# Kernel tuning notes

Hardware: AMD Instinct MI355X
Metric: run time of the kernel (lower is better)

## Reference

```python
import jax, jax.numpy as jnp
import numpy as np

D_MODEL = 1024
NUM_HEADS = 16
D_K = D_MODEL // NUM_HEADS
B, S = 2, 2048
NEG = -1e9


def setup_inputs() -> dict:
    key = jax.random.key(0)
    ks = jax.random.split(key, 12)
    scale = 1.0 / np.sqrt(D_MODEL)
    inp = {
        'q': jax.random.normal(ks[0], (B, S, D_MODEL), jnp.float32),
        'k': jax.random.normal(ks[1], (B, S, D_MODEL), jnp.float32),
        'v': jax.random.normal(ks[2], (B, S, D_MODEL), jnp.float32),
        'mask': jax.random.randint(ks[3], (1, 1, S, S), 0, 2, jnp.int32),
        'wq_w': jax.random.normal(ks[4], (D_MODEL, D_MODEL), jnp.float32) * scale,
        'wq_b': jnp.zeros((D_MODEL,), jnp.float32),
        'wk_w': jax.random.normal(ks[5], (D_MODEL, D_MODEL), jnp.float32) * scale,
        'wk_b': jnp.zeros((D_MODEL,), jnp.float32),
        'wv_w': jax.random.normal(ks[6], (D_MODEL, D_MODEL), jnp.float32) * scale,
        'wv_b': jnp.zeros((D_MODEL,), jnp.float32),
        'wo_w': jax.random.normal(ks[7], (D_MODEL, D_MODEL), jnp.float32) * scale,
        'wo_b': jnp.zeros((D_MODEL,), jnp.float32),
    }
    return inp


def _split_heads(x):
    # [B,S,D] -> [B,H,S,d_k]
    b, s, _ = x.shape
    return x.reshape(b, s, NUM_HEADS, D_K).transpose(0, 2, 1, 3)


def reference(q, k, v, mask, wq_w, wq_b, wk_w, wk_b, wv_w, wv_b, wo_w, wo_b):
    # torch Linear: y = x @ W.T + b
    qh = _split_heads(q @ wq_w.T + wq_b)
    kh = _split_heads(k @ wk_w.T + wk_b)
    vh = _split_heads(v @ wv_w.T + wv_b)
    scores = jnp.einsum('bhqd,bhkd->bhqk', qh, kh) / jnp.sqrt(jnp.float32(D_K))
    scores = jnp.where(mask == 0, jnp.float32(NEG), scores)
    attn = jax.nn.softmax(scores, axis=-1)  # dropout p=0 (eval): no-op
    x = jnp.einsum('bhqk,bhkd->bhqd', attn, vh)
    x = x.transpose(0, 2, 1, 3).reshape(q.shape[0], q.shape[1], D_MODEL)
    return x @ wo_w.T + wo_b
```

## Files before the change

kernel.cpp:

```cpp
#include <hip/hip_runtime.h>
#include <hip/hip_bf16.h>
#include <stdint.h>

#define S_LEN  2048
#define DMODEL 1024
#define NHEADS 16
#define DKH    64
#define KDIM   1024

typedef __bf16 bf16x8 __attribute__((ext_vector_type(8)));
typedef float  floatx4 __attribute__((ext_vector_type(4)));
typedef unsigned short ushort8v __attribute__((ext_vector_type(8)));

__device__ inline void gll16(const __bf16* g, const __bf16* l) {
    __builtin_amdgcn_global_load_lds(
        (const __attribute__((address_space(1))) void*)g,
        (__attribute__((address_space(3))) void*)l, 16, 0, 0);
}

__device__ inline float fast_exp2(float x) {
#if __has_builtin(__builtin_amdgcn_exp2f)
    return __builtin_amdgcn_exp2f(x);
#else
    return exp2f(x);
#endif
}

__device__ inline int bit_sign(uint32_t v, int idx) {
#if __has_builtin(__builtin_amdgcn_sbfe)
    return __builtin_amdgcn_sbfe((int)v, (uint32_t)idx, 1u);
#else
    return ((int)(v << (31 - idx))) >> 31;
#endif
}

__global__ __launch_bounds__(256) void prep_kernel(
    const float* __restrict__ q, const float* __restrict__ k, const float* __restrict__ v,
    const float* __restrict__ wq, const float* __restrict__ wk, const float* __restrict__ wv,
    const float* __restrict__ wo, __bf16* __restrict__ out,
    const int* __restrict__ M, uint64_t* __restrict__ P) {
    if (blockIdx.x < 8192) {
        const size_t i8 = ((size_t)blockIdx.x * 256 + threadIdx.x) * 8;
        const float* src;
        if (i8 < 4194304u)        src = q  + i8;
        else if (i8 < 8388608u)   src = k  + (i8 - 4194304u);
        else if (i8 < 12582912u)  src = v  + (i8 - 8388608u);
        else if (i8 < 13631488u)  src = wq + (i8 - 12582912u);
        else if (i8 < 14680064u)  src = wk + (i8 - 13631488u);
        else if (i8 < 15728640u)  src = wv + (i8 - 14680064u);
        else                      src = wo + (i8 - 15728640u);
        floatx4 a = *(const floatx4*)src;
        floatx4 b = *(const floatx4*)(src + 4);
        bf16x8 r;
#pragma unroll
        for (int i = 0; i < 4; ++i) { r[i] = (__bf16)a[i]; r[i + 4] = (__bf16)b[i]; }
        *(bf16x8*)(out + i8) = r;
    } else {
        const size_t i = ((size_t)(blockIdx.x - 8192)) * 256 + threadIdx.x;
        uint64_t bits = __ballot(M[i] != 0);
        if ((threadIdx.x & 63) == 0) P[i >> 6] = bits;
    }
}

__global__ __launch_bounds__(256, 5) void qkv_gemm(
    const __bf16* __restrict__ qb, const __bf16* __restrict__ kb, const __bf16* __restrict__ vb,
    const __bf16* __restrict__ wqw, const __bf16* __restrict__ wkw, const __bf16* __restrict__ wvw,
    const float* __restrict__ biasq, const float* __restrict__ biask, const float* __restrict__ biasv,
    __bf16* __restrict__ qh, __bf16* __restrict__ kh, __bf16* __restrict__ vt) {
    __shared__ __align__(16) __bf16 As[2 * 128 * 32];
    __shared__ __align__(16) __bf16 Bs[2 * 64 * 32];

    const int lane = threadIdx.x & 63;
    const int wave = threadIdx.x >> 6;
    const int quad = lane >> 4;
    const int l15  = lane & 15;

    const int bid = blockIdx.x;
    const int job = bid >> 9;
    const int tt  = bid & 511;
    const __bf16* A; const __bf16* Bm; const float* bias; __bf16* C;
    int bx, by, MODE;
    if (job == 0)      { A = qb;  Bm = wqw; bias = biasq; C = qh; bx = tt & 15; by = tt >> 4; MODE = 0; }
    else if (job == 1) { A = kb;  Bm = wkw; bias = biask; C = kh; bx = tt & 15; by = tt >> 4; MODE = 0; }
    else               { A = wvw; Bm = vb;  bias = biasv; C = vt; bx = tt & 63; by = tt >> 6; MODE = 1; }

    const int m_t = by * 128, n_t = bx * 64;
    const int m0w = (wave >> 1) * 64, n0w = (wave & 1) * 32;

    const int lrow = lane >> 2;
    const int scol = ((lane & 3) ^ (lrow & 3)) * 8;

    floatx4 acc[4][2];
#pragma unroll
    for (int i = 0; i < 4; ++i)
#pragma unroll
        for (int j = 0; j < 2; ++j)
            acc[i][j] = (floatx4){0.f, 0.f, 0.f, 0.f};

    for (int kk = 0; kk < KDIM; kk += 64) {
#pragma unroll
        for (int u = 0; u < 6; ++u) {
            const int pi = wave * 6 + u;
            if (pi < 16) {
                const int panel = pi >> 3, rb = pi & 7;
                gll16(A + (size_t)(m_t + rb * 16 + lrow) * KDIM + kk + panel * 32 + scol,
                      As + (panel * 128 + rb * 16) * 32);
            } else {
                const int qi = pi - 16, panel = qi >> 2, rb = qi & 3;
                gll16(Bm + (size_t)(n_t + rb * 16 + lrow) * KDIM + kk + panel * 32 + scol,
                      Bs + (panel * 64 + rb * 16) * 32);
            }
        }
        __syncthreads();
        const int cq = (quad ^ (l15 & 3)) * 8;
#pragma unroll
        for (int p = 0; p < 2; ++p) {
            bf16x8 af[4], bfr[2];
#pragma unroll
            for (int i = 0; i < 4; ++i)
                af[i] = *(const bf16x8*)(As + (p * 128 + m0w + i * 16 + l15) * 32 + cq);
#pragma unroll
            for (int j = 0; j < 2; ++j)
                bfr[j] = *(const bf16x8*)(Bs + (p * 64 + n0w + j * 16 + l15) * 32 + cq);
#pragma unroll
            for (int i = 0; i < 4; ++i)
#pragma unroll
                for (int j = 0; j < 2; ++j)
                    acc[i][j] = __builtin_amdgcn_mfma_f32_16x16x32_bf16(af[i], bfr[j], acc[i][j], 0, 0, 0);
        }
        __syncthreads();
    }

#pragma unroll
    for (int j = 0; j < 2; ++j) {
        const int n = n_t + n0w + j * 16 + l15;
        float bn = (MODE == 1) ? 0.f : bias[n];
#pragma unroll
        for (int i = 0; i < 4; ++i) {
#pragma unroll
            for (int r = 0; r < 4; ++r) {
                const int m = m_t + m0w + i * 16 + quad * 4 + r;
                float bv = (MODE == 1) ? bias[m] : bn;
                float v = acc[i][j][r] + bv;
                size_t off;
                if (MODE == 0) {
                    off = ((size_t)((m >> 11) * 16 + (n >> 6)) * 2048 + (m & 2047)) * 64 + (n & 63);
                } else {
                    off = ((size_t)((n >> 11) * 16 + (m >> 6)) * 64 + (m & 63)) * 2048 + (n & 2047);
                }
                C[off] = (__bf16)v;
            }
        }
    }
}

__global__ __launch_bounds__(256) void gemm_out(const __bf16* __restrict__ A,
                                                const __bf16* __restrict__ Bm,
                                                const float* __restrict__ bias,
                                                float* __restrict__ C) {
    __shared__ __align__(16) __bf16 As[2 * 128 * 32];
    __shared__ __align__(16) __bf16 Bs[2 * 64 * 32];

    const int lane = threadIdx.x & 63;
    const int wave = threadIdx.x >> 6;
    const int quad = lane >> 4;
    const int l15  = lane & 15;
    const int m_t = blockIdx.y * 128, n_t = blockIdx.x * 64;
    const int m0w = (wave >> 1) * 64, n0w = (wave & 1) * 32;

    const int lrow = lane >> 2;
    const int scol = ((lane & 3) ^ (lrow & 3)) * 8;

    floatx4 acc[4][2];
#pragma unroll
    for (int i = 0; i < 4; ++i)
#pragma unroll
        for (int j = 0; j < 2; ++j)
            acc[i][j] = (floatx4){0.f, 0.f, 0.f, 0.f};

    for (int kk = 0; kk < KDIM; kk += 64) {
#pragma unroll
        for (int u = 0; u < 6; ++u) {
            const int pi = wave * 6 + u;
            if (pi < 16) {
                const int panel = pi >> 3, rb = pi & 7;
                gll16(A + (size_t)(m_t + rb * 16 + lrow) * KDIM + kk + panel * 32 + scol,
                      As + (panel * 128 + rb * 16) * 32);
            } else {
                const int qi = pi - 16, panel = qi >> 2, rb = qi & 3;
                gll16(Bm + (size_t)(n_t + rb * 16 + lrow) * KDIM + kk + panel * 32 + scol,
                      Bs + (panel * 64 + rb * 16) * 32);
            }
        }
        __syncthreads();
        const int cq = (quad ^ (l15 & 3)) * 8;
#pragma unroll
        for (int p = 0; p < 2; ++p) {
            bf16x8 af[4], bfr[2];
#pragma unroll
            for (int i = 0; i < 4; ++i)
                af[i] = *(const bf16x8*)(As + (p * 128 + m0w + i * 16 + l15) * 32 + cq);
#pragma unroll
            for (int j = 0; j < 2; ++j)
                bfr[j] = *(const bf16x8*)(Bs + (p * 64 + n0w + j * 16 + l15) * 32 + cq);
#pragma unroll
            for (int i = 0; i < 4; ++i)
#pragma unroll
                for (int j = 0; j < 2; ++j)
                    acc[i][j] = __builtin_amdgcn_mfma_f32_16x16x32_bf16(af[i], bfr[j], acc[i][j], 0, 0, 0);
        }
        __syncthreads();
    }

#pragma unroll
    for (int j = 0; j < 2; ++j) {
        const int n = n_t + n0w + j * 16 + l15;
        const float bn = bias[n];
#pragma unroll
        for (int i = 0; i < 4; ++i)
#pragma unroll
            for (int r = 0; r < 4; ++r) {
                const int m = m_t + m0w + i * 16 + quad * 4 + r;
                C[(size_t)m * 1024 + n] = acc[i][j][r] + bn;
            }
    }
}

__global__ __launch_bounds__(256, 4) void attn_kernel(const __bf16* __restrict__ Qh,
                                                      const __bf16* __restrict__ Kh,
                                                      const __bf16* __restrict__ Vt,
                                                      const uint64_t* __restrict__ PM,
                                                      __bf16* __restrict__ X) {
    __shared__ __align__(16) __bf16 Ks[2][4096];
    __shared__ __align__(16) __bf16 Vs[2][4096];

    const int lane = threadIdx.x & 63;
    const int wave = threadIdx.x >> 6;
    const int quad = lane >> 4;
    const int l15  = lane & 15;
    const int l7   = l15 & 7;

    const int bid  = blockIdx.x;
    const int xcd  = bid & 7;
    const int slot = bid >> 3;
    const int grp  = xcd * 4 + (slot >> 5);
    const int qt   = slot & 31;
    const int b = grp >> 4, h = grp & 15;
    const int q0 = qt * 64 + wave * 16;

    const __bf16* Qb = Qh + (size_t)(b * NHEADS + h) * S_LEN * DKH;
    const __bf16* Kb = Kh + (size_t)(b * NHEADS + h) * S_LEN * DKH;
    const __bf16* Vb = Vt + (size_t)(b * NHEADS + h) * DKH * S_LEN;
    const uint64_t* pr = PM + (size_t)(q0 + l15) * (S_LEN / 64);

    const float cs = 0.18033688011112042f;
    const float MB = 4.0f;

    size_t offK[2], offV[2];
#pragma unroll
    for (int i = 0; i < 2; ++i) {
        const int s = wave * 128 + i * 64 + lane;
        const int r = s >> 3, cp = s & 7, c = cp ^ (r & 7);
        const int kr = (r >> 5) * 32 + ((r >> 4) & 1) * 4 + ((r >> 2) & 3) * 8 + (r & 3);
        offK[i] = (size_t)kr * DKH + c * 8;
        offV[i] = (size_t)r * S_LEN + c * 8;
    }

    bf16x8 qf[2];
#pragma unroll
    for (int c = 0; c < 2; ++c)
        qf[c] = *(const bf16x8*)(Qb + (size_t)(q0 + l15) * DKH + c * 32 + quad * 8);

    bf16x8 ones;
#pragma unroll
    for (int i = 0; i < 8; ++i) ones[i] = (__bf16)1.0f;

    floatx4 o[4], osum;
#pragma unroll
    for (int f = 0; f < 4; ++f) o[f] = (floatx4){0.f, 0.f, 0.f, 0.f};
    osum = (floatx4){0.f, 0.f, 0.f, 0.f};

    auto stage = [&](int p, int key0) {
#pragma unroll
        for (int i = 0; i < 2; ++i) {
            gll16(Kb + (size_t)key0 * DKH + offK[i], &Ks[p][(wave * 128 + i * 64) * 8]);
            gll16(Vb + key0 + offV[i],               &Vs[p][(wave * 128 + i * 64) * 8]);
        }
    };

    stage(0, 0);
    uint2 mwc = *(const uint2*)(pr);
    for (int kt = 0; kt < 32; ++kt) {
        const int p = kt & 1;
        __syncthreads();
        if (kt < 31) stage(p ^ 1, (kt + 1) * 64);
        const uint2 mw = mwc;
        if (kt < 31) mwc = *(const uint2*)(pr + kt + 1);

        bf16x8 kf[4][2];
#pragma unroll
        for (int t = 0; t < 4; ++t)
#pragma unroll
            for (int hh = 0; hh < 2; ++hh) {
                const int cp = ((hh * 4 + quad) ^ l7) * 8;
                kf[t][hh] = *(const bf16x8*)&Ks[p][(t * 16 + l15) * 64 + cp];
            }

        floatx4 st[4];
#pragma unroll
        for (int t = 0; t < 4; ++t) {
            floatx4 z = (floatx4){0.f, 0.f, 0.f, 0.f};
            z = __builtin_amdgcn_mfma_f32_16x16x32_bf16(kf[t][0], qf[0], z, 0, 0, 0);
            z = __builtin_amdgcn_mfma_f32_16x16x32_bf16(kf[t][1], qf[1], z, 0, 0, 0);
            st[t] = z;
        }

        bf16x8 pw[2];
#pragma unroll
        for (int w = 0; w < 2; ++w) {
            const uint32_t byte = (w ? mw.y : mw.x) >> (quad * 8);
            bf16x8 pb;
#pragma unroll
            for (int half = 0; half < 2; ++half) {
                const int t = w * 2 + half;
#pragma unroll
                for (int r = 0; r < 4; ++r) {
                    const int idx = half * 4 + r;
                    float e = fast_exp2(fmaf(st[t][r], cs, -MB));
                    const int sgn = bit_sign(byte, idx);
                    e = __builtin_bit_cast(float, __builtin_bit_cast(int, e) & sgn);
                    pb[half * 4 + r] = (__bf16)e;
                }
            }
            pw[w] = pb;
        }

#pragma unroll
        for (int w = 0; w < 2; ++w) {
            const int cp = ((w * 4 + quad) ^ l7) * 8;
#pragma unroll
            for (int f = 0; f < 4; ++f) {
                bf16x8 vf = *(const bf16x8*)&Vs[p][(f * 16 + l15) * 64 + cp];
                o[f] = __builtin_amdgcn_mfma_f32_16x16x32_bf16(vf, pw[w], o[f], 0, 0, 0);
            }
            osum = __builtin_amdgcn_mfma_f32_16x16x32_bf16(ones, pw[w], osum, 0, 0, 0);
        }
    }

    const float lsum = osum[0];
    const float inv = (lsum > 0.f) ? (1.f / lsum) : 0.f;

    __syncthreads();
    unsigned short* xw = (unsigned short*)&Ks[0][0] + wave * (16 * 80);
#pragma unroll
    for (int f = 0; f < 4; ++f)
#pragma unroll
        for (int r = 0; r < 4; ++r) {
            __bf16 bv = (__bf16)(o[f][r] * inv);
            xw[l15 * 80 + f * 16 + quad * 4 + r] = __builtin_bit_cast(unsigned short, bv);
        }
#pragma unroll
    for (int it = 0; it < 2; ++it) {
        const int ql = it * 8 + (lane >> 3);
        const int dseg = (lane & 7) * 8;
        ushort8v vv = *(const ushort8v*)&xw[ql * 80 + dseg];
        unsigned short* dst = (unsigned short*)X +
            (size_t)(b * S_LEN + q0 + ql) * DMODEL + h * DKH + dseg;
        *(ushort8v*)dst = vv;
    }
}

extern "C" void kernel_launch(void* const* d_in, const int* in_sizes, int n_in,
                              void* d_out, int out_size, void* d_ws, size_t ws_size,
                              hipStream_t stream) {
    const float* q   = (const float*)d_in[0];
    const float* k   = (const float*)d_in[1];
    const float* v   = (const float*)d_in[2];
    const int*   msk = (const int*)d_in[3];
    const float* wq  = (const float*)d_in[4];
    const float* wqb = (const float*)d_in[5];
    const float* wk  = (const float*)d_in[6];
    const float* wkb = (const float*)d_in[7];
    const float* wv  = (const float*)d_in[8];
    const float* wvb = (const float*)d_in[9];
    const float* wo  = (const float*)d_in[10];
    const float* wob = (const float*)d_in[11];

    char* ws = (char*)d_ws;
    __bf16*   qh   = (__bf16*)(ws);
    __bf16*   kh   = (__bf16*)(ws + 8388608);
    __bf16*   vt   = (__bf16*)(ws + 16777216);
    uint64_t* pm   = (uint64_t*)(ws + 25165824);
    __bf16*   cb   = (__bf16*)(ws + 25690112);
    __bf16*   qb   = cb;
    __bf16*   kb   = cb + 4194304;
    __bf16*   vb   = cb + 8388608;
    __bf16*   wqbf = cb + 12582912;
    __bf16*   wkbf = cb + 13631488;
    __bf16*   wvbf = cb + 14680064;
    __bf16*   wobf = cb + 15728640;
    __bf16*   xa   = qb;

    prep_kernel<<<24576, 256, 0, stream>>>(q, k, v, wq, wk, wv, wo, cb, msk, pm);
    qkv_gemm<<<1536, 256, 0, stream>>>(qb, kb, vb, wqbf, wkbf, wvbf, wqb, wkb, wvb, qh, kh, vt);
    attn_kernel<<<1024, 256, 0, stream>>>(qh, kh, vt, pm, xa);
    gemm_out<<<dim3(16, 32), 256, 0, stream>>>(xa, wobf, wob, (float*)d_out);
}
```

Baseline: 266.8 us.

## Rewrite attention inner loop with 32x32x16 MFMA and split-key waves

```diff
diff --git a/kernel.cpp b/kernel.cpp
--- a/kernel.cpp
+++ b/kernel.cpp
@@ -9,8 +9,12 @@
 #define KDIM   1024
 
 typedef __bf16 bf16x8 __attribute__((ext_vector_type(8)));
+typedef __bf16 bf16x2 __attribute__((ext_vector_type(2)));
 typedef float  floatx4 __attribute__((ext_vector_type(4)));
+typedef float  floatx16 __attribute__((ext_vector_type(16)));
 typedef unsigned short ushort8v __attribute__((ext_vector_type(8)));
+typedef unsigned int  uint32x2 __attribute__((ext_vector_type(2)));
+typedef unsigned int  uint32x4 __attribute__((ext_vector_type(4)));
 
 __device__ inline void gll16(const __bf16* g, const __bf16* l) {
     __builtin_amdgcn_global_load_lds(
@@ -32,6 +36,10 @@
 #else
     return ((int)(v << (31 - idx))) >> 31;
 #endif
+}
+
+__device__ inline void plswap(uint32_t& a, uint32_t& b) {
+    asm volatile("v_permlane32_swap_b32 %0, %1" : "+v"(a), "+v"(b));
 }
 
 __global__ __launch_bounds__(256) void prep_kernel(
@@ -236,9 +244,10 @@
 
     const int lane = threadIdx.x & 63;
     const int wave = threadIdx.x >> 6;
-    const int quad = lane >> 4;
-    const int l15  = lane & 15;
-    const int l7   = l15 & 7;
+    const int l31  = lane & 31;
+    const int hi   = lane >> 5;
+    const int kh   = wave & 1;
+    const int qhf  = wave >> 1;
 
     const int bid  = blockIdx.x;
     const int xcd  = bid & 7;
@@ -246,127 +255,148 @@
     const int grp  = xcd * 4 + (slot >> 5);
     const int qt   = slot & 31;
     const int b = grp >> 4, h = grp & 15;
-    const int q0 = qt * 64 + wave * 16;
+    const int qw = qt * 64 + qhf * 32;
 
     const __bf16* Qb = Qh + (size_t)(b * NHEADS + h) * S_LEN * DKH;
     const __bf16* Kb = Kh + (size_t)(b * NHEADS + h) * S_LEN * DKH;
     const __bf16* Vb = Vt + (size_t)(b * NHEADS + h) * DKH * S_LEN;
-    const uint64_t* pr = PM + (size_t)(q0 + l15) * (S_LEN / 64);
+    const uint64_t* pr = PM + (size_t)(qw + l31) * (S_LEN / 64);
 
     const float cs = 0.18033688011112042f;
-    const float MB = 4.0f;
-
-    size_t offK[2], offV[2];
+
+    uint32_t offK[2], offV[2];
 #pragma unroll
     for (int i = 0; i < 2; ++i) {
-        const int s = wave * 128 + i * 64 + lane;
-        const int r = s >> 3, cp = s & 7, c = cp ^ (r & 7);
-        const int kr = (r >> 5) * 32 + ((r >> 4) & 1) * 4 + ((r >> 2) & 3) * 8 + (r & 3);
-        offK[i] = (size_t)kr * DKH + c * 8;
-        offV[i] = (size_t)r * S_LEN + c * 8;
-    }
-
-    bf16x8 qf[2];
-#pragma unroll
-    for (int c = 0; c < 2; ++c)
-        qf[c] = *(const bf16x8*)(Qb + (size_t)(q0 + l15) * DKH + c * 32 + quad * 8);
-
-    bf16x8 ones;
-#pragma unroll
-    for (int i = 0; i < 8; ++i) ones[i] = (__bf16)1.0f;
-
-    floatx4 o[4], osum;
-#pragma unroll
-    for (int f = 0; f < 4; ++f) o[f] = (floatx4){0.f, 0.f, 0.f, 0.f};
-    osum = (floatx4){0.f, 0.f, 0.f, 0.f};
+        const int pi  = wave * 2 + i;
+        const int khs = pi >> 2, kss = pi & 3;
+        offK[i] = (uint32_t)((khs * 32 + l31) * DKH + kss * 16 + hi * 8);
+        const int dts = pi >> 2, khv = (pi >> 1) & 1, cv = pi & 1;
+        offV[i] = (uint32_t)((dts * 32 + l31) * S_LEN + khv * 32 + cv * 16 + hi * 8);
+    }
 
     auto stage = [&](int p, int key0) {
 #pragma unroll
         for (int i = 0; i < 2; ++i) {
-            gll16(Kb + (size_t)key0 * DKH + offK[i], &Ks[p][(wave * 128 + i * 64) * 8]);
-            gll16(Vb + key0 + offV[i],               &Vs[p][(wave * 128 + i * 64) * 8]);
+            gll16(Kb + (size_t)key0 * DKH + offK[i], Ks[p] + (wave * 2 + i) * 512);
+            gll16(Vb + (size_t)key0 + offV[i],       Vs[p] + (wave * 2 + i) * 512);
         }
     };
 
+    bf16x8 qf[4];
+#pragma unroll
+    for (int ks = 0; ks < 4; ++ks)
+        qf[ks] = *(const bf16x8*)(Qb + (size_t)(qw + l31) * DKH + ks * 16 + hi * 8);
+
+    floatx16 o0, o1;
+#pragma unroll
+    for (int i = 0; i < 16; ++i) { o0[i] = 0.f; o1[i] = 0.f; }
+    float ls0 = 0.f;
+
+    const __bf16* Kl = &Ks[0][kh * 2048 + lane * 8];
+    const __bf16* Vl = &Vs[0][kh * 1024 + lane * 8];
+
     stage(0, 0);
-    uint2 mwc = *(const uint2*)(pr);
+    uint64_t mwc = pr[0];
+
     for (int kt = 0; kt < 32; ++kt) {
         const int p = kt & 1;
         __syncthreads();
         if (kt < 31) stage(p ^ 1, (kt + 1) * 64);
-        const uint2 mw = mwc;
-        if (kt < 31) mwc = *(const uint2*)(pr + kt + 1);
-
-        bf16x8 kf[4][2];
-#pragma unroll
-        for (int t = 0; t < 4; ++t)
-#pragma unroll
-            for (int hh = 0; hh < 2; ++hh) {
-                const int cp = ((hh * 4 + quad) ^ l7) * 8;
-                kf[t][hh] = *(const bf16x8*)&Ks[p][(t * 16 + l15) * 64 + cp];
-            }
-
-        floatx4 st[4];
-#pragma unroll
-        for (int t = 0; t < 4; ++t) {
-            floatx4 z = (floatx4){0.f, 0.f, 0.f, 0.f};
-            z = __builtin_amdgcn_mfma_f32_16x16x32_bf16(kf[t][0], qf[0], z, 0, 0, 0);
-            z = __builtin_amdgcn_mfma_f32_16x16x32_bf16(kf[t][1], qf[1], z, 0, 0, 0);
-            st[t] = z;
-        }
-
-        bf16x8 pw[2];
-#pragma unroll
-        for (int w = 0; w < 2; ++w) {
-            const uint32_t byte = (w ? mw.y : mw.x) >> (quad * 8);
-            bf16x8 pb;
-#pragma unroll
-            for (int half = 0; half < 2; ++half) {
-                const int t = w * 2 + half;
-#pragma unroll
-                for (int r = 0; r < 4; ++r) {
-                    const int idx = half * 4 + r;
-                    float e = fast_exp2(fmaf(st[t][r], cs, -MB));
-                    const int sgn = bit_sign(byte, idx);
-                    e = __builtin_bit_cast(float, __builtin_bit_cast(int, e) & sgn);
-                    pb[half * 4 + r] = (__bf16)e;
-                }
-            }
-            pw[w] = pb;
-        }
-
-#pragma unroll
-        for (int w = 0; w < 2; ++w) {
-            const int cp = ((w * 4 + quad) ^ l7) * 8;
-#pragma unroll
-            for (int f = 0; f < 4; ++f) {
-                bf16x8 vf = *(const bf16x8*)&Vs[p][(f * 16 + l15) * 64 + cp];
-                o[f] = __builtin_amdgcn_mfma_f32_16x16x32_bf16(vf, pw[w], o[f], 0, 0, 0);
-            }
-            osum = __builtin_amdgcn_mfma_f32_16x16x32_bf16(ones, pw[w], osum, 0, 0, 0);
-        }
-    }
-
-    const float lsum = osum[0];
-    const float inv = (lsum > 0.f) ? (1.f / lsum) : 0.f;
+        const uint64_t mw = mwc;
+        if (kt < 31) mwc = pr[kt + 1];
+
+        const __bf16* Kp = Kl + p * 4096;
+        const __bf16* Vp = Vl + p * 4096;
+
+        floatx16 st;
+#pragma unroll
+        for (int i = 0; i < 16; ++i) st[i] = 0.f;
+#pragma unroll
+        for (int ks = 0; ks < 4; ++ks) {
+            bf16x8 kf = *(const bf16x8*)(Kp + ks * 512);
+            st = __builtin_amdgcn_mfma_f32_32x32x16_bf16(kf, qf[ks], st, 0, 0, 0);
+        }
+
+        const uint32_t w32 = (uint32_t)(kh ? (mw >> 32) : mw);
+        const uint32_t wsh = w32 >> (hi * 4);
+
+        float e[16];
+#pragma unroll
+        for (int r = 0; r < 16; ++r) {
+            const int cpos = (r & 3) + 8 * (r >> 2);
+            float v = fast_exp2(st[r] * cs);
+            const int sgn = bit_sign(wsh, cpos);
+            e[r] = __builtin_bit_cast(float, __builtin_bit_cast(int, v) & sgn);
+        }
+        ls0 += (((e[0] + e[1]) + (e[2] + e[3])) + ((e[4] + e[5]) + (e[6] + e[7])))
+             + (((e[8] + e[9]) + (e[10] + e[11])) + ((e[12] + e[13]) + (e[14] + e[15])));
+
+        uint32_t w[8];
+#pragma unroll
+        for (int r2 = 0; r2 < 8; ++r2) {
+            bf16x2 pp; pp[0] = (__bf16)e[2 * r2]; pp[1] = (__bf16)e[2 * r2 + 1];
+            w[r2] = __builtin_bit_cast(uint32_t, pp);
+        }
+        plswap(w[0], w[2]);
+        plswap(w[1], w[3]);
+        plswap(w[4], w[6]);
+        plswap(w[5], w[7]);
+        uint32x4 f0 = {w[0], w[1], w[2], w[3]};
+        uint32x4 f1 = {w[4], w[5], w[6], w[7]};
+        bf16x8 pf0 = __builtin_bit_cast(bf16x8, f0);
+        bf16x8 pf1 = __builtin_bit_cast(bf16x8, f1);
+
+        bf16x8 vf;
+        vf = *(const bf16x8*)(Vp + 0 * 2048 + 0 * 512);
+        o0 = __builtin_amdgcn_mfma_f32_32x32x16_bf16(vf, pf0, o0, 0, 0, 0);
+        vf = *(const bf16x8*)(Vp + 0 * 2048 + 1 * 512);
+        o0 = __builtin_amdgcn_mfma_f32_32x32x16_bf16(vf, pf1, o0, 0, 0, 0);
+        vf = *(const bf16x8*)(Vp + 1 * 2048 + 0 * 512);
+        o1 = __builtin_amdgcn_mfma_f32_32x32x16_bf16(vf, pf0, o1, 0, 0, 0);
+        vf = *(const bf16x8*)(Vp + 1 * 2048 + 1 * 512);
+        o1 = __builtin_amdgcn_mfma_f32_32x32x16_bf16(vf, pf1, o1, 0, 0, 0);
+    }
+
+    float lsum2 = ls0 + __shfl_xor(ls0, 32);
 
     __syncthreads();
-    unsigned short* xw = (unsigned short*)&Ks[0][0] + wave * (16 * 80);
-#pragma unroll
-    for (int f = 0; f < 4; ++f)
-#pragma unroll
-        for (int r = 0; r < 4; ++r) {
-            __bf16 bv = (__bf16)(o[f][r] * inv);
-            xw[l15 * 80 + f * 16 + quad * 4 + r] = __builtin_bit_cast(unsigned short, bv);
-        }
-#pragma unroll
-    for (int it = 0; it < 2; ++it) {
-        const int ql = it * 8 + (lane >> 3);
-        const int dseg = (lane & 7) * 8;
-        ushort8v vv = *(const ushort8v*)&xw[ql * 80 + dseg];
-        unsigned short* dst = (unsigned short*)X +
-            (size_t)(b * S_LEN + q0 + ql) * DMODEL + h * DKH + dseg;
-        *(ushort8v*)dst = vv;
+    float* red  = (float*)&Ks[0][0];
+    float* redl = (float*)&Vs[0][0];
+    if (kh == 1) {
+#pragma unroll
+        for (int g = 0; g < 16; ++g) red[(qhf * 32 + g) * 64 + lane] = o0[g];
+#pragma unroll
+        for (int g = 0; g < 16; ++g) red[(qhf * 32 + 16 + g) * 64 + lane] = o1[g];
+        redl[qhf * 64 + lane] = lsum2;
+    }
+    __syncthreads();
+    if (kh == 0) {
+        const float lt  = lsum2 + redl[qhf * 64 + lane];
+        const float inv = (lt > 0.f) ? (1.f / lt) : 0.f;
+        unsigned short* xp = (unsigned short*)X +
+            (size_t)(b * S_LEN + qw + l31) * DMODEL + h * DKH;
+#pragma unroll
+        for (int g = 0; g < 4; ++g) {
+            float va = (o0[g * 4 + 0] + red[(qhf * 32 + g * 4 + 0) * 64 + lane]) * inv;
+            float vb = (o0[g * 4 + 1] + red[(qhf * 32 + g * 4 + 1) * 64 + lane]) * inv;
+            float vc = (o0[g * 4 + 2] + red[(qhf * 32 + g * 4 + 2) * 64 + lane]) * inv;
+            float vd = (o0[g * 4 + 3] + red[(qhf * 32 + g * 4 + 3) * 64 + lane]) * inv;
+            bf16x2 pa; pa[0] = (__bf16)va; pa[1] = (__bf16)vb;
+            bf16x2 pb; pb[0] = (__bf16)vc; pb[1] = (__bf16)vd;
+            uint32x2 wv = {__builtin_bit_cast(uint32_t, pa), __builtin_bit_cast(uint32_t, pb)};
+            *(uint32x2*)(xp + g * 8 + hi * 4) = wv;
+        }
+#pragma unroll
+        for (int g = 0; g < 4; ++g) {
+            float va = (o1[g * 4 + 0] + red[(qhf * 32 + 16 + g * 4 + 0) * 64 + lane]) * inv;
+            float vb = (o1[g * 4 + 1] + red[(qhf * 32 + 16 + g * 4 + 1) * 64 + lane]) * inv;
+            float vc = (o1[g * 4 + 2] + red[(qhf * 32 + 16 + g * 4 + 2) * 64 + lane]) * inv;
+            float vd = (o1[g * 4 + 3] + red[(qhf * 32 + 16 + g * 4 + 3) * 64 + lane]) * inv;
+            bf16x2 pa; pa[0] = (__bf16)va; pa[1] = (__bf16)vb;
+            bf16x2 pb; pb[0] = (__bf16)vc; pb[1] = (__bf16)vd;
+            uint32x2 wv = {__builtin_bit_cast(uint32_t, pa), __builtin_bit_cast(uint32_t, pb)};
+            *(uint32x2*)(xp + 32 + g * 8 + hi * 4) = wv;
+        }
     }
 }
 
```

Measured after the change: 285.8 us. 1.07x slower.
